# Kernel tuning notes

Hardware: AMD Instinct MI355X
Metric: run time of the kernel (lower is better)

The kernel has to match this reference:

```python
import jax, jax.numpy as jnp
import numpy as np

B, T, C, H = 2, 2048, 1024, 16
D = C // H  # head dim = 64


def setup_inputs() -> dict:
    key = jax.random.key(0)
    ks = jax.random.split(key, 9)
    s = 1.0 / np.sqrt(C)
    inp = {
        "x": jax.random.normal(ks[0], (B, T, C), dtype=jnp.float32),
        # causal mask, broadcast over batch and heads
        "att_mask": jnp.tril(jnp.ones((T, T), dtype=jnp.int32))[None, None, :, :],
        "wq": jax.random.uniform(ks[1], (C, C), jnp.float32, -s, s),
        "bq": jax.random.uniform(ks[2], (C,), jnp.float32, -s, s),
        "wk": jax.random.uniform(ks[3], (C, C), jnp.float32, -s, s),
        "bk": jax.random.uniform(ks[4], (C,), jnp.float32, -s, s),
        "wv": jax.random.uniform(ks[5], (C, C), jnp.float32, -s, s),
        "bv": jax.random.uniform(ks[6], (C,), jnp.float32, -s, s),
        "wp": jax.random.uniform(ks[7], (C, C), jnp.float32, -s, s),
        "bp": jax.random.uniform(ks[8], (C,), jnp.float32, -s, s),
    }
    return inp


def _split_heads(t):
    # [B,T,C] -> [B,H,T,D]
    return t.reshape(B, T, H, D).transpose(0, 2, 1, 3)


def reference(x, att_mask, wq, bq, wk, bk, wv, bv, wp, bp):
    # torch nn.Linear: y = x @ W.T + b
    q = _split_heads(x @ wq.T + bq)
    k = _split_heads(x @ wk.T + bk)
    v = _split_heads(x @ wv.T + bv)
    scale = 1.0 / np.sqrt(D).astype(np.float32)
    att = jnp.einsum("bhtd,bhsd->bhts", q, k) * scale  # [B,H,T,T]
    neg_inf = jnp.asarray(-jnp.inf, dtype=att.dtype)
    att = jnp.where(att_mask == 0, neg_inf, att)
    att = jax.nn.softmax(att, axis=-1)
    att = jnp.where(att_mask == 0, jnp.asarray(0.0, att.dtype), att)
    y = jnp.einsum("bhts,bhsd->bhtd", att, v)  # [B,H,T,D]
    y = y.transpose(0, 2, 1, 3).reshape(B, T, C)
    # attn_pdrop / resid_pdrop are None -> no dropout, single proj
    return y @ wp.T + bp
```

## Files before the change

kernel.cpp:

```cpp
#include <hip/hip_runtime.h>
#include <math.h>

#define Bz 2
#define Tz 2048
#define Cz 1024
#define Hz 16
#define Dz 64
#define Mz (Bz*Tz)

typedef short bf16x8 __attribute__((ext_vector_type(8)));
typedef short bf16x4 __attribute__((ext_vector_type(4)));
typedef float f32x4  __attribute__((ext_vector_type(4)));
typedef float f32x16 __attribute__((ext_vector_type(16)));

__device__ __forceinline__ unsigned short f2bf(float f) {
    union { float f; unsigned u; } v; v.f = f;
    unsigned r = v.u + 0x7fffu + ((v.u >> 16) & 1u);
    return (unsigned short)(r >> 16);
}

__device__ __forceinline__ float fexp2(float x) {
#if __has_builtin(__builtin_amdgcn_exp2f)
    return __builtin_amdgcn_exp2f(x);
#else
    return exp2f(x);
#endif
}

__device__ __forceinline__ void pl32swap(unsigned &a, unsigned &b) {
    asm("v_permlane32_swap_b32 %0, %1" : "+v"(a), "+v"(b));
}

#define GLD16(gp, lp) __builtin_amdgcn_global_load_lds( \
    (const __attribute__((address_space(1))) unsigned int*)(gp), \
    (__attribute__((address_space(3))) unsigned int*)(lp), 16, 0, 0)


__global__ __launch_bounds__(256)
void cast_all(const float* __restrict__ x,  const float* __restrict__ wq,
              const float* __restrict__ wk, const float* __restrict__ wv,
              const float* __restrict__ wp,
              unsigned short* __restrict__ xb, unsigned short* __restrict__ wqkvb,
              unsigned short* __restrict__ wpb)
{
    const size_t M1 = 1u << 20;
    size_t i = ((size_t)blockIdx.x * 256 + threadIdx.x) * 4;
    const float* s; unsigned short* d; size_t o;
    int reg = (int)(i >> 20);
    if      (reg < 4)  { s = x;  d = xb;           o = i;          }
    else if (reg == 4) { s = wq; d = wqkvb;        o = i - 4 * M1; }
    else if (reg == 5) { s = wk; d = wqkvb + M1;   o = i - 5 * M1; }
    else if (reg == 6) { s = wv; d = wqkvb + 2*M1; o = i - 6 * M1; }
    else               { s = wp; d = wpb;          o = i - 7 * M1; }
    float4 v = *(const float4*)&s[o];
    ushort4 u;
    u.x = f2bf(v.x); u.y = f2bf(v.y); u.z = f2bf(v.z); u.w = f2bf(v.w);
    *(ushort4*)&d[o] = u;
}

template<int AI, int EPI>
__global__ __launch_bounds__(256)
void mfma_gemm(const unsigned short* __restrict__ A, const unsigned short* __restrict__ W,
               const float* __restrict__ b0, const float* __restrict__ b1,
               const float* __restrict__ b2,
               void* out0, void* out1, void* out2)
{
    __shared__ unsigned short As[2][AI * 32][64];
    __shared__ unsigned short Bs[2][128][64];
    const int t = threadIdx.x, w = t >> 6, l = t & 63;
    const int m0 = blockIdx.y * (AI * 32);
    const int n0 = blockIdx.x * 128;
    const int wr = w >> 1, wc = w & 1;
    const int g = l >> 4, ln = l & 15;
    const int lrow  = l >> 3;
    const int lcolb = (l & 7) ^ lrow;
    const int xm = ln & 7;

    f32x4 acc[AI][4];
#pragma unroll
    for (int i = 0; i < AI; ++i)
#pragma unroll
        for (int j = 0; j < 4; ++j) acc[i][j] = (f32x4){0.f, 0.f, 0.f, 0.f};

    auto stage = [&](int bsel, int k0) {
#pragma unroll
        for (int p = 0; p < AI; ++p) {
            const int rb = (w * AI + p) * 8;
            GLD16(A + (size_t)(m0 + rb + lrow) * 1024 + k0 + lcolb * 8,
                  (unsigned short*)As[bsel] + rb * 64);
        }
#pragma unroll
        for (int p = 0; p < 4; ++p) {
            const int rb = (w * 4 + p) * 8;
            GLD16(W + (size_t)(n0 + rb + lrow) * 1024 + k0 + lcolb * 8,
                  (unsigned short*)Bs[bsel] + rb * 64);
        }
    };

    stage(0, 0);
    for (int it = 0; it < 16; ++it) {
        stage((it + 1) & 1, (it < 15 ? it + 1 : 15) * 64);
        if constexpr (AI == 4) asm volatile("s_waitcnt vmcnt(8)" ::: "memory");
        else                   asm volatile("s_waitcnt vmcnt(6)" ::: "memory");
        __builtin_amdgcn_s_barrier();
        __builtin_amdgcn_sched_barrier(0);
        const int cb = it & 1;
#pragma unroll
        for (int kk = 0; kk < 2; ++kk) {
            bf16x8 af[AI], bf[4];
#pragma unroll
            for (int i = 0; i < AI; ++i)
                af[i] = *(const bf16x8*)&As[cb][wr * (AI * 16) + i * 16 + ln][((kk * 4 + g) ^ xm) * 8];
#pragma unroll
            for (int j = 0; j < 4; ++j)
                bf[j] = *(const bf16x8*)&Bs[cb][wc * 64 + j * 16 + ln][((kk * 4 + g) ^ xm) * 8];
#pragma unroll
            for (int i = 0; i < AI; ++i)
#pragma unroll
                for (int j = 0; j < 4; ++j)
                    acc[i][j] = __builtin_amdgcn_mfma_f32_16x16x32_bf16(af[i], bf[j], acc[i][j], 0, 0, 0);
        }
        asm volatile("s_waitcnt lgkmcnt(0)" ::: "memory");
        __builtin_amdgcn_s_barrier();
    }
    asm volatile("s_waitcnt vmcnt(0)" ::: "memory");
    __syncthreads();

    if (EPI == 0) {
        const float QSC = 0.125f * 1.44269504088896f;
        const int gn0  = n0 + wc * 64;
        const int sel  = gn0 >> 10;
        const int rem0 = gn0 & 1023;
        const int h    = rem0 >> 6;
        const float* bsrc = (sel == 0) ? b0 : ((sel == 1) ? b1 : b2);
        float bj[4];
#pragma unroll
        for (int j = 0; j < 4; ++j) bj[j] = bsrc[rem0 + j * 16 + ln];

        if (sel == 2) {
            unsigned short* vd = (unsigned short*)out2;
#pragma unroll
            for (int i = 0; i < AI; ++i)
#pragma unroll
                for (int j = 0; j < 4; ++j) {
                    const int dd  = j * 16 + ln;
                    const int gm0 = m0 + wr * (AI * 16) + i * 16 + g * 4;
                    const int b = gm0 >> 11, t0 = gm0 & 2047;
                    const int tile = t0 >> 6, tt = t0 & 63;
                    const int ks = tt >> 4, hi2 = (tt >> 3) & 1, e = tt & 7;
                    const int j32 = dd >> 5, qc = dd & 31;
                    ushort4 pk;
                    pk.x = f2bf(acc[i][j][0] + bj[j]); pk.y = f2bf(acc[i][j][1] + bj[j]);
                    pk.z = f2bf(acc[i][j][2] + bj[j]); pk.w = f2bf(acc[i][j][3] + bj[j]);
                    const size_t off = (size_t)(b * Hz + h) * (Tz * Dz)
                                     + tile * 4096 + ((j32 * 4 + ks) * 2 + hi2) * 256 + qc * 8 + e;
                    *(ushort4*)&vd[off] = pk;
                }
        } else {
            unsigned short* dst = (sel == 0) ? (unsigned short*)out0 : (unsigned short*)out1;
            unsigned short* scrw = ((unsigned short*)As) + w * (16 * 72);
            const int row16 = l & 15, ch = l >> 4;
#pragma unroll
            for (int i = 0; i < AI; ++i) {
#pragma unroll
                for (int j = 0; j < 4; ++j)
#pragma unroll
                    for (int r = 0; r < 4; ++r) {
                        float v = acc[i][j][r] + bj[j];
                        if (sel == 0) v *= QSC;
                        scrw[(g * 4 + r) * 72 + j * 16 + ln] = f2bf(v);
                    }
                const int gm = m0 + wr * (AI * 16) + i * 16 + row16;
                const int b = gm >> 11, tt = gm & 2047;
                bf16x8 v0 = *(const bf16x8*)&scrw[row16 * 72 + ch * 8];
                bf16x8 v1 = *(const bf16x8*)&scrw[row16 * 72 + (ch + 4) * 8];
                if (sel == 0) {
                    const size_t base = (size_t)((b * Hz + h) * Tz + tt) * Dz;
                    *(bf16x8*)&dst[base + ch * 8] = v0;
                    *(bf16x8*)&dst[base + (ch + 4) * 8] = v1;
                } else {
                    const int tile = tt >> 6, rr = tt & 63;
                    const int kb32 = rr >> 5, qc = rr & 31;
                    const size_t tb = (size_t)(b * Hz + h) * (Tz * Dz) + tile * 4096;
                    *(bf16x8*)&dst[tb + (kb32 * 8 + ch) * 256 + qc * 8]       = v0;
                    *(bf16x8*)&dst[tb + (kb32 * 8 + ch + 4) * 256 + qc * 8]   = v1;
                }
            }
        }
    } else {
        float* od = (float*)out0;
#pragma unroll
        for (int i = 0; i < AI; ++i)
#pragma unroll
            for (int j = 0; j < 4; ++j) {
                const int gn = n0 + wc * 64 + j * 16 + ln;
                const float bjv = b0[gn];
#pragma unroll
                for (int r = 0; r < 4; ++r) {
                    const int gm = m0 + wr * (AI * 16) + i * 16 + g * 4 + r;
                    od[(size_t)gm * 1024 + gn] = acc[i][j][r] + bjv;
                }
            }
    }
}

__global__ __launch_bounds__(256, 3)
void attn_wave(const unsigned short* __restrict__ Q, const unsigned short* __restrict__ K,
               const unsigned short* __restrict__ Vt, unsigned short* __restrict__ AO)
{
    __shared__ float Om[2][32][65];
    __shared__ float Lw[2][32];

    const int t = threadIdx.x, w = t >> 6, l = t & 63;
    const int qc = l & 31;
    const int hi = l >> 5;
    const int hi8 = hi << 3, hi4 = hi << 2;
    const int bh = blockIdx.x;
    const int chunk = 63 - (int)blockIdx.y;
    const int q0 = chunk * 32;
    const size_t hb = (size_t)bh * Tz * Dz;

    const int ntiles = (q0 >> 6) + 1;
    const int it0 = (w * ntiles) >> 2;
    const int it1 = ((w + 1) * ntiles) >> 2;

    bf16x8 qf[4];
#pragma unroll
    for (int kb = 0; kb < 4; ++kb)
        qf[kb] = *(const bf16x8*)&Q[hb + (size_t)(q0 + qc) * Dz + kb * 16 + hi8];

    f32x16 o0, o1;
    float lrs = 0.f;
#pragma unroll
    for (int r = 0; r < 16; ++r) { o0[r] = 0.f; o1[r] = 0.f; }

    const int ktLast = (q0 >> 6) << 6;
    const float SMAX = 20.f;

    for (int it = it0; it < it1; ++it) {
        const int kt = it * 64;
        const size_t tb = hb + (size_t)it * 4096;

        bf16x8 kf[2][4];
#pragma unroll
        for (int kb32 = 0; kb32 < 2; ++kb32)
#pragma unroll
            for (int kb = 0; kb < 4; ++kb)
                kf[kb32][kb] = *(const bf16x8*)&K[tb + (size_t)((kb32 * 4 + kb) * 64 + l) * 8];

        f32x16 s2[2];
#pragma unroll
        for (int r = 0; r < 16; ++r) { s2[0][r] = 0.f; s2[1][r] = 0.f; }
        __builtin_amdgcn_s_setprio(1);
#pragma unroll
        for (int kb32 = 0; kb32 < 2; ++kb32)
#pragma unroll
            for (int kb = 0; kb < 4; ++kb)
                s2[kb32] = __builtin_amdgcn_mfma_f32_32x32x16_bf16(kf[kb32][kb], qf[kb], s2[kb32], 0, 0, 0);
        __builtin_amdgcn_s_setprio(0);

        bf16x8 vf[2][4];
#pragma unroll
        for (int j32 = 0; j32 < 2; ++j32)
#pragma unroll
            for (int ks = 0; ks < 4; ++ks)
                vf[j32][ks] = *(const bf16x8*)&Vt[tb + (size_t)((j32 * 4 + ks) * 64 + l) * 8];

        if (kt == ktLast) {
            const int qv = q0 + qc;
#pragma unroll
            for (int kb32 = 0; kb32 < 2; ++kb32)
#pragma unroll
                for (int r = 0; r < 16; ++r) {
                    const int key = kt + kb32 * 32 + (r & 3) + 8 * (r >> 2) + hi4;
                    if (key > qv) s2[kb32][r] = -__builtin_inff();
                }
        }

        bf16x8 pf[4];
#pragma unroll
        for (int kb32 = 0; kb32 < 2; ++kb32) {
            unsigned pk[4][2];
#pragma unroll
            for (int sg = 0; sg < 4; ++sg)
#pragma unroll
                for (int u = 0; u < 2; ++u) {
                    const float e0 = fexp2(s2[kb32][sg * 4 + 2 * u]     - SMAX);
                    const float e1 = fexp2(s2[kb32][sg * 4 + 2 * u + 1] - SMAX);
                    lrs += e0 + e1;
                    pk[sg][u] = __builtin_amdgcn_perm(__float_as_uint(e1), __float_as_uint(e0), 0x07060302u);
                }
#pragma unroll
            for (int kb16 = 0; kb16 < 2; ++kb16) {
                unsigned a0 = pk[2 * kb16][0], b0 = pk[2 * kb16 + 1][0];
                unsigned a1 = pk[2 * kb16][1], b1 = pk[2 * kb16 + 1][1];
                pl32swap(a0, b0);
                pl32swap(a1, b1);
                union { unsigned u[4]; bf16x8 v; } P;
                P.u[0] = a0; P.u[1] = a1; P.u[2] = b0; P.u[3] = b1;
                pf[kb32 * 2 + kb16] = P.v;
            }
        }

        __builtin_amdgcn_s_setprio(1);
#pragma unroll
        for (int ks = 0; ks < 4; ++ks) {
            o0 = __builtin_amdgcn_mfma_f32_32x32x16_bf16(pf[ks], vf[0][ks], o0, 0, 0, 0);
            o1 = __builtin_amdgcn_mfma_f32_32x32x16_bf16(pf[ks], vf[1][ks], o1, 0, 0, 0);
        }
        __builtin_amdgcn_s_setprio(0);
    }

    {
        unsigned a = __float_as_uint(lrs), b = a;
        pl32swap(a, b);
        lrs += hi ? __uint_as_float(a) : __uint_as_float(b);
    }

    if (w & 1) {
        const int buf = w >> 1;
#pragma unroll
        for (int r = 0; r < 16; ++r) {
            const int row = (r & 3) + 8 * (r >> 2) + hi4;
            Om[buf][row][qc]      = o0[r];
            Om[buf][row][32 + qc] = o1[r];
        }
        if (hi == 0) Lw[buf][qc] = lrs;
    }
    __syncthreads();
    if (!(w & 1)) {
        const int buf = w >> 1;
#pragma unroll
        for (int r = 0; r < 16; ++r) {
            const int row = (r & 3) + 8 * (r >> 2) + hi4;
            o0[r] += Om[buf][row][qc];
            o1[r] += Om[buf][row][32 + qc];
        }
        lrs += Lw[buf][qc];
    }
    __syncthreads();
    if (w == 2) {
#pragma unroll
        for (int r = 0; r < 16; ++r) {
            const int row = (r & 3) + 8 * (r >> 2) + hi4;
            Om[0][row][qc]      = o0[r];
            Om[0][row][32 + qc] = o1[r];
        }
        if (hi == 0) Lw[0][qc] = lrs;
    }
    __syncthreads();
    if (w == 0) {
        const int b = bh >> 4, h = bh & 15;
        const float lsum = lrs + Lw[0][qc];
#pragma unroll
        for (int r = 0; r < 16; ++r) {
            const int row = (r & 3) + 8 * (r >> 2) + hi4;
            const float ov0 = o0[r] + Om[0][row][qc];
            const float ov1 = o1[r] + Om[0][row][32 + qc];
            const unsigned lq = __builtin_amdgcn_ds_bpermute(row << 2, __float_as_uint(lsum));
            const float linv = 1.f / __uint_as_float(lq);
            const size_t ob = (size_t)(b * Tz + q0 + row) * Cz + h * Dz + qc;
            AO[ob]      = f2bf(ov0 * linv);
            AO[ob + 32] = f2bf(ov1 * linv);
        }
    }
}

extern "C" void kernel_launch(void* const* d_in, const int* in_sizes, int n_in,
                              void* d_out, int out_size, void* d_ws, size_t ws_size,
                              hipStream_t stream) {
    const float* x  = (const float*)d_in[0];
    const float* wq = (const float*)d_in[2];
    const float* bq = (const float*)d_in[3];
    const float* wk = (const float*)d_in[4];
    const float* bk = (const float*)d_in[5];
    const float* wv = (const float*)d_in[6];
    const float* bv = (const float*)d_in[7];
    const float* wp = (const float*)d_in[8];
    const float* bp = (const float*)d_in[9];
    float* out = (float*)d_out;

    char* wsb = (char*)d_ws;
    unsigned short* xb    = (unsigned short*)(wsb);
    unsigned short* wqkvb = (unsigned short*)(wsb + (8u  << 20));
    unsigned short* wpb   = (unsigned short*)(wsb + (14u << 20));
    unsigned short* Qb    = (unsigned short*)(wsb + (17u << 20));
    unsigned short* Kb    = (unsigned short*)(wsb + (25u << 20));
    unsigned short* Vtb   = (unsigned short*)(wsb + (33u << 20));
    unsigned short* AOb   = (unsigned short*)(wsb + (41u << 20));

    hipLaunchKernelGGL(cast_all, dim3(8192), dim3(256), 0, stream,
                       x, wq, wk, wv, wp, xb, wqkvb, wpb);

    hipLaunchKernelGGL((mfma_gemm<4, 0>), dim3(24, 32), dim3(256), 0, stream,
                       xb, wqkvb, bq, bk, bv, Qb, Kb, Vtb);

    hipLaunchKernelGGL(attn_wave, dim3(32, 64), dim3(256), 0, stream,
                       Qb, Kb, Vtb, AOb);

    hipLaunchKernelGGL((mfma_gemm<2, 1>), dim3(8, 64), dim3(256), 0, stream,
                       AOb, wpb, bp, bp, bp, out, nullptr, nullptr);
}
```

Baseline: 186.7 us.

## Fuse cast, QKV GEMM, attention and projection into one cooperative persistent kernel

Merges the four separate launches into a single cooperative kernel of 512 (or 256) persistent blocks. The blocks loop over the cast elements, GEMM tiles and attention tasks, with grid-wide syncs between phases. The aim is to remove per-launch overhead and inter-kernel gaps. In exchange, every phase now runs with a fixed 64KB shared allocation and no attention-specific launch bounds, which may lower occupancy. It also adds grid-sync cost and tail imbalance in the 768-tile GEMM phase. A fallback path with separate kernels is kept.

```diff
diff --git a/kernel.cpp b/kernel.cpp
--- a/kernel.cpp
+++ b/kernel.cpp
@@ -1,22 +1,24 @@
 #include <hip/hip_runtime.h>
+#include <hip/hip_cooperative_groups.h>
 #include <math.h>
+
+namespace cg = cooperative_groups;
 
 #define Bz 2
 #define Tz 2048
 #define Cz 1024
 #define Hz 16
 #define Dz 64
-#define Mz (Bz*Tz)
-
+
+typedef unsigned short us;
 typedef short bf16x8 __attribute__((ext_vector_type(8)));
-typedef short bf16x4 __attribute__((ext_vector_type(4)));
 typedef float f32x4  __attribute__((ext_vector_type(4)));
 typedef float f32x16 __attribute__((ext_vector_type(16)));
 
-__device__ __forceinline__ unsigned short f2bf(float f) {
+__device__ __forceinline__ us f2bf(float f) {
     union { float f; unsigned u; } v; v.f = f;
     unsigned r = v.u + 0x7fffu + ((v.u >> 16) & 1u);
-    return (unsigned short)(r >> 16);
+    return (us)(r >> 16);
 }
 
 __device__ __forceinline__ float fexp2(float x) {
@@ -35,17 +37,20 @@
     (const __attribute__((address_space(1))) unsigned int*)(gp), \
     (__attribute__((address_space(3))) unsigned int*)(lp), 16, 0, 0)
 
-
-__global__ __launch_bounds__(256)
-void cast_all(const float* __restrict__ x,  const float* __restrict__ wq,
-              const float* __restrict__ wk, const float* __restrict__ wv,
-              const float* __restrict__ wp,
-              unsigned short* __restrict__ xb, unsigned short* __restrict__ wqkvb,
-              unsigned short* __restrict__ wpb)
+__device__ __forceinline__ void gsync() {
+    __threadfence();
+    cg::this_grid().sync();
+}
+
+
+__device__ __forceinline__ void cast_one(size_t q,
+    const float* __restrict__ x,  const float* __restrict__ wq,
+    const float* __restrict__ wk, const float* __restrict__ wv,
+    const float* __restrict__ wp, us* xb, us* wqkvb, us* wpb)
 {
     const size_t M1 = 1u << 20;
-    size_t i = ((size_t)blockIdx.x * 256 + threadIdx.x) * 4;
-    const float* s; unsigned short* d; size_t o;
+    size_t i = q * 4;
+    const float* s; us* d; size_t o;
     int reg = (int)(i >> 20);
     if      (reg < 4)  { s = x;  d = xb;           o = i;          }
     else if (reg == 4) { s = wq; d = wqkvb;        o = i - 4 * M1; }
@@ -59,23 +64,26 @@
 }
 
 template<int AI, int EPI>
-__global__ __launch_bounds__(256)
-void mfma_gemm(const unsigned short* __restrict__ A, const unsigned short* __restrict__ W,
-               const float* __restrict__ b0, const float* __restrict__ b1,
-               const float* __restrict__ b2,
-               void* out0, void* out1, void* out2)
-{
-    __shared__ unsigned short As[2][AI * 32][64];
-    __shared__ unsigned short Bs[2][128][64];
+__device__ void gemm_tile(char* smem, int bx, int by,
+                          const us* __restrict__ A, const us* __restrict__ W,
+                          const float* __restrict__ b0, const float* __restrict__ b1,
+                          const float* __restrict__ b2,
+                          void* out0, void* out1, void* out2)
+{
+    us (*As)[AI * 32][64] = (us (*)[AI * 32][64])smem;
+    us (*Bs)[128][64]     = (us (*)[128][64])(smem + (size_t)2 * AI * 32 * 64 * 2);
+
     const int t = threadIdx.x, w = t >> 6, l = t & 63;
-    const int m0 = blockIdx.y * (AI * 32);
-    const int n0 = blockIdx.x * 128;
+    const int m0 = by * (AI * 32);
+    const int n0 = bx * 128;
     const int wr = w >> 1, wc = w & 1;
     const int g = l >> 4, ln = l & 15;
     const int lrow  = l >> 3;
     const int lcolb = (l & 7) ^ lrow;
     const int xm = ln & 7;
 
+    __syncthreads();
+
     f32x4 acc[AI][4];
 #pragma unroll
     for (int i = 0; i < AI; ++i)
@@ -87,13 +95,13 @@
         for (int p = 0; p < AI; ++p) {
             const int rb = (w * AI + p) * 8;
             GLD16(A + (size_t)(m0 + rb + lrow) * 1024 + k0 + lcolb * 8,
-                  (unsigned short*)As[bsel] + rb * 64);
+                  (us*)As[bsel] + rb * 64);
         }
 #pragma unroll
         for (int p = 0; p < 4; ++p) {
             const int rb = (w * 4 + p) * 8;
             GLD16(W + (size_t)(n0 + rb + lrow) * 1024 + k0 + lcolb * 8,
-                  (unsigned short*)Bs[bsel] + rb * 64);
+                  (us*)Bs[bsel] + rb * 64);
         }
     };
 
@@ -138,7 +146,7 @@
         for (int j = 0; j < 4; ++j) bj[j] = bsrc[rem0 + j * 16 + ln];
 
         if (sel == 2) {
-            unsigned short* vd = (unsigned short*)out2;
+            us* vd = (us*)out2;
 #pragma unroll
             for (int i = 0; i < AI; ++i)
 #pragma unroll
@@ -157,8 +165,8 @@
                     *(ushort4*)&vd[off] = pk;
                 }
         } else {
-            unsigned short* dst = (sel == 0) ? (unsigned short*)out0 : (unsigned short*)out1;
-            unsigned short* scrw = ((unsigned short*)As) + w * (16 * 72);
+            us* dst = (sel == 0) ? (us*)out0 : (us*)out1;
+            us* scrw = (us*)smem + w * (16 * 72);
             const int row16 = l & 15, ch = l >> 4;
 #pragma unroll
             for (int i = 0; i < AI; ++i) {
@@ -204,19 +212,17 @@
     }
 }
 
-__global__ __launch_bounds__(256, 3)
-void attn_wave(const unsigned short* __restrict__ Q, const unsigned short* __restrict__ K,
-               const unsigned short* __restrict__ Vt, unsigned short* __restrict__ AO)
-{
-    __shared__ float Om[2][32][65];
-    __shared__ float Lw[2][32];
+__device__ void attn_task(char* smem, int bh, int chunk,
+                          const us* __restrict__ Q, const us* __restrict__ K,
+                          const us* __restrict__ Vt, us* __restrict__ AO)
+{
+    float (*Om)[32][65] = (float (*)[32][65])smem;
+    float* Lw = (float*)(smem + 16640);
 
     const int t = threadIdx.x, w = t >> 6, l = t & 63;
     const int qc = l & 31;
     const int hi = l >> 5;
     const int hi8 = hi << 3, hi4 = hi << 2;
-    const int bh = blockIdx.x;
-    const int chunk = 63 - (int)blockIdx.y;
     const int q0 = chunk * 32;
     const size_t hb = (size_t)bh * Tz * Dz;
 
@@ -317,6 +323,7 @@
         lrs += hi ? __uint_as_float(a) : __uint_as_float(b);
     }
 
+    __syncthreads();
     if (w & 1) {
         const int buf = w >> 1;
 #pragma unroll
@@ -325,7 +332,7 @@
             Om[buf][row][qc]      = o0[r];
             Om[buf][row][32 + qc] = o1[r];
         }
-        if (hi == 0) Lw[buf][qc] = lrs;
+        if (hi == 0) Lw[buf * 32 + qc] = lrs;
     }
     __syncthreads();
     if (!(w & 1)) {
@@ -336,7 +343,7 @@
             o0[r] += Om[buf][row][qc];
             o1[r] += Om[buf][row][32 + qc];
         }
-        lrs += Lw[buf][qc];
+        lrs += Lw[buf * 32 + qc];
     }
     __syncthreads();
     if (w == 2) {
@@ -346,12 +353,12 @@
             Om[0][row][qc]      = o0[r];
             Om[0][row][32 + qc] = o1[r];
         }
-        if (hi == 0) Lw[0][qc] = lrs;
+        if (hi == 0) Lw[qc] = lrs;
     }
     __syncthreads();
     if (w == 0) {
         const int b = bh >> 4, h = bh & 15;
-        const float lsum = lrs + Lw[0][qc];
+        const float lsum = lrs + Lw[qc];
 #pragma unroll
         for (int r = 0; r < 16; ++r) {
             const int row = (r & 3) + 8 * (r >> 2) + hi4;
@@ -364,6 +371,61 @@
             AO[ob + 32] = f2bf(ov1 * linv);
         }
     }
+    __syncthreads();
+}
+
+__global__ __launch_bounds__(256)
+void fused_all(const float* __restrict__ x,  const float* __restrict__ wq,
+               const float* __restrict__ wk, const float* __restrict__ wv,
+               const float* __restrict__ wp,
+               const float* __restrict__ bq, const float* __restrict__ bk,
+               const float* __restrict__ bv, const float* __restrict__ bp,
+               us* xb, us* wqkvb, us* wpb, us* Qb, us* Kb, us* Vtb, us* AOb,
+               float* out)
+{
+    __shared__ __align__(16) char smem[65536];
+    const int bid = blockIdx.x, tid = threadIdx.x, G = gridDim.x;
+
+    for (size_t q = (size_t)bid * 256 + tid; q < (size_t)(1u << 21); q += (size_t)G * 256)
+        cast_one(q, x, wq, wk, wv, wp, xb, wqkvb, wpb);
+    gsync();
+
+    for (int tile = bid; tile < 768; tile += G)
+        gemm_tile<4, 0>(smem, tile % 24, tile / 24, xb, wqkvb, bq, bk, bv, Qb, Kb, Vtb);
+    gsync();
+
+    for (int task = bid; task < 2048; task += G)
+        attn_task(smem, task & 31, 63 - (task >> 5), Qb, Kb, Vtb, AOb);
+    gsync();
+
+    for (int tile = bid; tile < 512; tile += G)
+        gemm_tile<2, 1>(smem, tile & 7, tile >> 3, AOb, wpb, bp, bp, bp, out, nullptr, nullptr);
+}
+
+__global__ __launch_bounds__(256)
+void cast_fb(const float* __restrict__ x,  const float* __restrict__ wq,
+             const float* __restrict__ wk, const float* __restrict__ wv,
+             const float* __restrict__ wp, us* xb, us* wqkvb, us* wpb)
+{
+    cast_one((size_t)blockIdx.x * 256 + threadIdx.x, x, wq, wk, wv, wp, xb, wqkvb, wpb);
+}
+
+template<int AI, int EPI>
+__global__ __launch_bounds__(256)
+void gemm_fb(const us* __restrict__ A, const us* __restrict__ W,
+             const float* __restrict__ b0, const float* __restrict__ b1,
+             const float* __restrict__ b2, void* o0, void* o1, void* o2)
+{
+    __shared__ __align__(16) char smem[(2 * AI * 32 * 64 + 2 * 128 * 64) * 2];
+    gemm_tile<AI, EPI>(smem, blockIdx.x, blockIdx.y, A, W, b0, b1, b2, o0, o1, o2);
+}
+
+__global__ __launch_bounds__(256)
+void attn_fb(const us* __restrict__ Q, const us* __restrict__ K,
+             const us* __restrict__ Vt, us* __restrict__ AO)
+{
+    __shared__ __align__(16) char smem[17408];
+    attn_task(smem, blockIdx.x, 63 - (int)blockIdx.y, Q, K, Vt, AO);
 }
 
 extern "C" void kernel_launch(void* const* d_in, const int* in_sizes, int n_in,
@@ -381,23 +443,43 @@
     float* out = (float*)d_out;
 
     char* wsb = (char*)d_ws;
-    unsigned short* xb    = (unsigned short*)(wsb);
-    unsigned short* wqkvb = (unsigned short*)(wsb + (8u  << 20));
-    unsigned short* wpb   = (unsigned short*)(wsb + (14u << 20));
-    unsigned short* Qb    = (unsigned short*)(wsb + (17u << 20));
-    unsigned short* Kb    = (unsigned short*)(wsb + (25u << 20));
-    unsigned short* Vtb   = (unsigned short*)(wsb + (33u << 20));
-    unsigned short* AOb   = (unsigned short*)(wsb + (41u << 20));
-
-    hipLaunchKernelGGL(cast_all, dim3(8192), dim3(256), 0, stream,
+    us* xb    = (us*)(wsb);
+    us* wqkvb = (us*)(wsb + (8u  << 20));
+    us* wpb   = (us*)(wsb + (14u << 20));
+    us* Qb    = (us*)(wsb + (17u << 20));
+    us* Kb    = (us*)(wsb + (25u << 20));
+    us* Vtb   = (us*)(wsb + (33u << 20));
+    us* AOb   = (us*)(wsb + (41u << 20));
+
+    void* args[] = { (void*)&x, (void*)&wq, (void*)&wk, (void*)&wv, (void*)&wp,
+                     (void*)&bq, (void*)&bk, (void*)&bv, (void*)&bp,
+                     (void*)&xb, (void*)&wqkvb, (void*)&wpb,
+                     (void*)&Qb, (void*)&Kb, (void*)&Vtb, (void*)&AOb,
+                     (void*)&out };
+
+    static int mode = -1;
+    if (mode < 0) {
+        if (hipLaunchCooperativeKernel((const void*)fused_all, dim3(512), dim3(256),
+                                       args, 0, stream) == hipSuccess) { mode = 2; return; }
+        (void)hipGetLastError();
+        if (hipLaunchCooperativeKernel((const void*)fused_all, dim3(256), dim3(256),
+                                       args, 0, stream) == hipSuccess) { mode = 1; return; }
+        (void)hipGetLastError();
+        mode = 0;
+    } else if (mode == 2) {
+        hipLaunchCooperativeKernel((const void*)fused_all, dim3(512), dim3(256), args, 0, stream);
+        return;
+    } else if (mode == 1) {
+        hipLaunchCooperativeKernel((const void*)fused_all, dim3(256), dim3(256), args, 0, stream);
+        return;
+    }
+
+    hipLaunchKernelGGL(cast_fb, dim3(8192), dim3(256), 0, stream,
                        x, wq, wk, wv, wp, xb, wqkvb, wpb);
-
-    hipLaunchKernelGGL((mfma_gemm<4, 0>), dim3(24, 32), dim3(256), 0, stream,
+    hipLaunchKernelGGL((gemm_fb<4, 0>), dim3(24, 32), dim3(256), 0, stream,
                        xb, wqkvb, bq, bk, bv, Qb, Kb, Vtb);
-
-    hipLaunchKernelGGL(attn_wave, dim3(32, 64), dim3(256), 0, stream,
+    hipLaunchKernelGGL(attn_fb, dim3(32, 64), dim3(256), 0, stream,
                        Qb, Kb, Vtb, AOb);
-
-    hipLaunchKernelGGL((mfma_gemm<2, 1>), dim3(8, 64), dim3(256), 0, stream,
+    hipLaunchKernelGGL((gemm_fb<2, 1>), dim3(8, 64), dim3(256), 0, stream,
                        AOb, wpb, bp, bp, bp, out, nullptr, nullptr);
 }
```

Measured after the change: 221.1 us. 18.4% more time.
